# Kernel optimization log

Measured on AMD Instinct MI355X. Metric: run time of the kernel, lower is better.

## Reference

```python
import jax, jax.numpy as jnp
import numpy as np

EPS = 1e-6
ROPE_THETA = 10000.0


def rmsnorm(x, w):
    return x * jax.lax.rsqrt(jnp.mean(x * x, axis=-1, keepdims=True) + EPS) * w


def rope(q, k, seq_len, head_dim):
    # rotate-half RoPE. q,k: [b, h, s, d]
    half = head_dim // 2
    inv_freq = 1.0 / (ROPE_THETA ** (jnp.arange(0, half, dtype=jnp.float32) / half))
    t = jnp.arange(seq_len, dtype=jnp.float32)
    freqs = jnp.outer(t, inv_freq)                      # [s, d/2]
    cos = jnp.concatenate([jnp.cos(freqs)] * 2, axis=-1)  # [s, d]
    sin = jnp.concatenate([jnp.sin(freqs)] * 2, axis=-1)

    def rot(x):
        x1, x2 = x[..., :half], x[..., half:]
        return jnp.concatenate([-x2, x1], axis=-1)

    return q * cos + rot(q) * sin, k * cos + rot(k) * sin


def setup_inputs() -> dict:
    key = jax.random.key(0)
    ks = jax.random.split(key, 8)
    B, S, D, E, F = 4, 2048, 1024, 8, 4096
    sd = 0.02
    return {
        "x": jax.random.normal(ks[0], (B, S, D), dtype=jnp.float32),
        "mapped_tokens": jax.random.randint(ks[1], (B, S), 0, E, dtype=jnp.int32),
        "rms1_w": jnp.ones((D,), dtype=jnp.float32),
        "wqkv": jax.random.normal(ks[2], (D, 3 * D), dtype=jnp.float32) * sd,
        "wo": jax.random.normal(ks[3], (D, D), dtype=jnp.float32) * sd,
        "rms2_w": jnp.ones((D,), dtype=jnp.float32),
        "w1": jax.random.normal(ks[4], (E, D, F), dtype=jnp.float32) * sd,
        "w2": jax.random.normal(ks[5], (E, F, D), dtype=jnp.float32) * sd,
    }


def attention(x, wqkv, wo, num_heads=16):
    B, S, D = x.shape
    hd = D // num_heads
    qkv = x @ wqkv                                       # [b, s, 3D]
    q, k, v = jnp.split(qkv, 3, axis=-1)
    def heads(t):
        return t.reshape(B, S, num_heads, hd).transpose(0, 2, 1, 3)  # [b,h,s,d]
    q, k, v = heads(q), heads(k), heads(v)
    q, k = rope(q, k, S, hd)
    scores = jnp.einsum("bhqd,bhkd->bhqk", q, k) / jnp.sqrt(jnp.float32(hd))
    causal = jnp.tril(jnp.ones((S, S), dtype=bool))
    scores = jnp.where(causal, scores, jnp.finfo(scores.dtype).min)
    attn = jax.nn.softmax(scores, axis=-1)
    out = jnp.einsum("bhqk,bhkd->bhqd", attn, v)
    out = out.transpose(0, 2, 1, 3).reshape(B, S, D)
    return out @ wo


def moe_hash_ffn(x, mapped_tokens, w1, w2):
    # hash-routed MoE: each token goes to exactly one expert given by mapped_tokens
    B, S, D = x.shape
    E = w1.shape[0]
    xf = x.reshape(B * S, D)
    mt = mapped_tokens.reshape(B * S)
    out = jnp.zeros_like(xf)
    for e in range(E):  # small fixed expert count
        y = jax.nn.gelu(xf @ w1[e]) @ w2[e]
        out = out + jnp.where((mt == e)[:, None], y, 0.0)
    return out.reshape(B, S, D)


def reference(x, mapped_tokens, rms1_w, wqkv, wo, rms2_w, w1, w2):
    h = x + attention(rmsnorm(x, rms1_w), wqkv, wo)
    out = h + moe_hash_ffn(rmsnorm(h, rms2_w), mapped_tokens, w1, w2)
    return out
```

## Files before the change

kernel.cpp:

```cpp
#include <hip/hip_runtime.h>
#include <hip/hip_bf16.h>
#include <stdint.h>

typedef __hip_bfloat16 bf16;
typedef __attribute__((ext_vector_type(8))) short bf16x8;
typedef __attribute__((ext_vector_type(4))) float f32x4;
typedef __attribute__((ext_vector_type(16))) float f32x16;
typedef unsigned int u32;

static constexpr int Bsz = 4, S = 2048, D = 1024, E = 8, F = 4096, NH = 16, HD = 64;
static constexpr int TOK = Bsz * S;
static constexpr int SLOTS = TOK + E * 128;

#define DEV __device__ __forceinline__

DEV void async16(const bf16* g, bf16* l) {
  __builtin_amdgcn_global_load_lds((const __attribute__((address_space(1))) u32*)g,
                                   (__attribute__((address_space(3))) u32*)l, 16, 0, 0);
}

DEV u32 lds_off(const bf16* p) {
  return (u32)(uintptr_t)(__attribute__((address_space(3))) bf16*)p;
}

DEV bf16x8 dsr128(u32 addr) {
  bf16x8 d;
  asm volatile("ds_read_b128 %0, %1" : "=v"(d) : "v"(addr));
  return d;
}

DEV float gelu_fast(float x) {
  const float z = 0.7978845608028654f * (x + 0.044715f * x * x * x);
  return x / (1.f + __expf(-2.f * z));
}


__global__ void cvt_transpose(const float* __restrict__ in, bf16* __restrict__ out, int R, int C) {
  __shared__ float t[64][65];
  const size_t zoff = (size_t)blockIdx.z * R * C;
  const int c0 = blockIdx.x * 64, r0 = blockIdx.y * 64;
  const int tid = threadIdx.x;
  const int lrow = tid >> 4, lcol = (tid & 15) * 4;
#pragma unroll
  for (int p = 0; p < 4; ++p) {
    const int r = lrow + p * 16;
    const float4 v = *(const float4*)(in + zoff + (size_t)(r0 + r) * C + c0 + lcol);
    t[r][lcol] = v.x; t[r][lcol + 1] = v.y; t[r][lcol + 2] = v.z; t[r][lcol + 3] = v.w;
  }
  __syncthreads();
  const int ow = tid >> 3, je = (tid & 7) * 8;
#pragma unroll
  for (int p = 0; p < 2; ++p) {
    const int oc = ow + p * 32;
    union { bf16x8 v; bf16 b[8]; } o8;
#pragma unroll
    for (int j = 0; j < 8; ++j) o8.b[j] = __float2bfloat16(t[je + j][oc]);
    *(bf16x8*)(out + zoff + (size_t)(c0 + oc) * R + r0 + je) = o8.v;
  }
}

__global__ void rope_tables(float* __restrict__ cosT, float* __restrict__ sinT) {
  const int s = blockIdx.x * 2 + (threadIdx.x >> 5);
  const int i = threadIdx.x & 31;
  const float inv_freq = powf(10000.f, -(float)i / 32.f);
  const float ang = (float)s * inv_freq;
  cosT[s * 32 + i] = cosf(ang);
  sinT[s * 32 + i] = sinf(ang);
}

__global__ void rmsnorm_k(const float* __restrict__ x, const float* __restrict__ w, bf16* __restrict__ out) {
  const size_t row = blockIdx.x;
  const int tid = threadIdx.x;
  const float4 v = *(const float4*)(x + row * D + tid * 4);
  float ss = v.x * v.x + v.y * v.y + v.z * v.z + v.w * v.w;
#pragma unroll
  for (int off = 1; off < 64; off <<= 1) ss += __shfl_xor(ss, off);
  __shared__ float red[4];
  if ((tid & 63) == 0) red[tid >> 6] = ss;
  __syncthreads();
  const float inv = rsqrtf((red[0] + red[1] + red[2] + red[3]) * (1.f / D) + 1e-6f);
  const float4 wv = *(const float4*)(w + tid * 4);
  union { ushort4 u; bf16 b[4]; } o;
  o.b[0] = __float2bfloat16(v.x * inv * wv.x);
  o.b[1] = __float2bfloat16(v.y * inv * wv.y);
  o.b[2] = __float2bfloat16(v.z * inv * wv.z);
  o.b[3] = __float2bfloat16(v.w * inv * wv.w);
  *(ushort4*)((unsigned short*)out + row * D + tid * 4) = o.u;
}

__global__ void route_init(int* counts, int* cursors, int* perm) {
  const int i = blockIdx.x * 256 + threadIdx.x;
  if (i < E) { counts[i] = 0; cursors[i] = 0; }
  if (i < SLOTS) perm[i] = -1;
}
__global__ void route_count(const int* __restrict__ mt, int* counts) {
  const int i = blockIdx.x * 256 + threadIdx.x;
  if (i < TOK) atomicAdd(&counts[mt[i]], 1);
}
__global__ void route_offsets(const int* __restrict__ counts, int* aoff) {
  if (threadIdx.x == 0) {
    int off = 0; aoff[0] = 0;
    for (int e = 0; e < E; ++e) { off += (counts[e] + 127) & ~127; aoff[e + 1] = off; }
  }
}
__global__ void route_scatter(const int* __restrict__ mt, const int* __restrict__ aoff,
                              int* cursors, int* perm) {
  const int i = blockIdx.x * 256 + threadIdx.x;
  if (i < TOK) { const int e = mt[i]; perm[aoff[e] + atomicAdd(&cursors[e], 1)] = i; }
}

__global__ __launch_bounds__(512) void qkv8p(
    const bf16* __restrict__ A, const bf16* __restrict__ Bt,
    const float* __restrict__ c_t, const float* __restrict__ s_t,
    bf16* __restrict__ o_q, bf16* __restrict__ o_k, bf16* __restrict__ o_v) {
  constexpr int K = 1024, NT = K / 64;
  __shared__ __align__(16) bf16 LA[2][256 * 64];
  __shared__ __align__(16) bf16 LB[2][256 * 64];
  const int tid = threadIdx.x;
  const int lane = tid & 63, wv = tid >> 6;
  const int wm = wv >> 2, wn = wv & 3;
  const int rl = lane & 15, kg = lane >> 4;
  const int gx = gridDim.x;
  const int nwg = gx * gridDim.y;
  int bid = blockIdx.y * gx + blockIdx.x;
  bid = (bid & 7) * (nwg >> 3) + (bid >> 3);
  const int nbase = (bid % gx) * 256, mbase = (bid / gx) * 256;
  f32x4 acc[8][4] = {};
  const int srow = tid >> 3;
  const int sc = (tid & 7) ^ ((srow >> 1) & 7);
  const bf16* Ag = A + (size_t)(mbase + srow) * K + sc * 8;
  const bf16* Bg = Bt + (size_t)(nbase + srow) * K + sc * 8;

  auto stage = [&](int t, int h) {
    const int buf = t & 1;
    const int mat = h >> 1, rh = h & 1;
    const bf16* src = (mat ? Bg : Ag) + (size_t)(rh * 128) * K + t * 64;
    bf16* dst = (mat ? &LB[buf][0] : &LA[buf][0]) + rh * 128 * 64 + tid * 8;
    async16(src, dst);
    async16(src + (size_t)64 * K, dst + 64 * 64);
  };

  bf16x8 bfr[4];
  auto phaseC = [&](int t, int ks, int mih, bool loadB) {
    const int buf = t & 1;
    const u32 ab = lds_off(&LA[buf][0]);
    const u32 bb = lds_off(&LB[buf][0]);
    bf16x8 af[4];
#pragma unroll
    for (int mi = 0; mi < 4; ++mi) {
      const int row = wm * 128 + mih * 64 + mi * 16 + rl;
      const u32 ph = (u32)((ks * 4 + kg) ^ ((row >> 1) & 7));
      af[mi] = dsr128(ab + (u32)row * 128 + ph * 16);
    }
    if (loadB) {
#pragma unroll
      for (int ni = 0; ni < 4; ++ni) {
        const int row = wn * 64 + ni * 16 + rl;
        const u32 ph = (u32)((ks * 4 + kg) ^ ((row >> 1) & 7));
        bfr[ni] = dsr128(bb + (u32)row * 128 + ph * 16);
      }
    }
    asm volatile("s_waitcnt lgkmcnt(0)" ::: "memory");
    __builtin_amdgcn_sched_barrier(0);
    __builtin_amdgcn_s_setprio(1);
#pragma unroll
    for (int mi = 0; mi < 4; ++mi)
#pragma unroll
      for (int ni = 0; ni < 4; ++ni)
        acc[mih * 4 + mi][ni] =
            __builtin_amdgcn_mfma_f32_16x16x32_bf16(af[mi], bfr[ni], acc[mih * 4 + mi][ni], 0, 0, 0);
    __builtin_amdgcn_s_setprio(0);
  };

  stage(0, 0); stage(0, 1); stage(0, 2); stage(0, 3);
  for (int t = 0; t < NT; ++t) {
    const bool more = (t + 1 < NT);
#pragma unroll
    for (int p = 0; p < 4; ++p) {
      if (p == 0) {
        if (more) {
          stage(t + 1, 0);
          asm volatile("s_waitcnt vmcnt(2)" ::: "memory");
        } else {
          asm volatile("s_waitcnt vmcnt(0)" ::: "memory");
        }
        __builtin_amdgcn_s_barrier();
        __builtin_amdgcn_sched_barrier(0);
      } else if (more) {
        stage(t + 1, p);
      }
      phaseC(t, p >> 1, p & 1, (p & 1) == 0);
      __builtin_amdgcn_s_barrier();
      __builtin_amdgcn_sched_barrier(0);
    }
  }

  const int colbase = nbase + wn * 64;
  const int part = colbase >> 10;
  const int head = (colbase & 1023) >> 6;
#pragma unroll
  for (int ai = 0; ai < 8; ++ai) {
    const int rowoff = (ai >> 2) * 64 + (ai & 3) * 16;
#pragma unroll
    for (int r = 0; r < 4; ++r) {
      const int grow = mbase + wm * 128 + rowoff + kg * 4 + r;
      const int bb = grow >> 11, sp = grow & (S - 1);
      if (part == 2) {
#pragma unroll
        for (int ni = 0; ni < 4; ++ni) {
          const int d = ni * 16 + rl;
          o_v[((size_t)(bb * NH + head) * HD + d) * S + sp] = __float2bfloat16(acc[ai][ni][r]);
        }
      } else {
        bf16* dst = (part == 0) ? o_q : o_k;
        const size_t base = ((size_t)(bb * NH + head) * S + sp) * HD;
#pragma unroll
        for (int np = 0; np < 2; ++np) {
          const int i = np * 16 + rl;
          const float c = c_t[sp * 32 + i];
          const float sn = s_t[sp * 32 + i];
          const float lo = acc[ai][np][r];
          const float hi = acc[ai][np + 2][r];
          dst[base + i] = __float2bfloat16(lo * c - hi * sn);
          dst[base + i + 32] = __float2bfloat16(hi * c + lo * sn);
        }
      }
    }
  }
}

template <int EPI, int BM>
__global__ __launch_bounds__(2 * BM) void gemm_bt(
    const bf16* __restrict__ A, const bf16* __restrict__ Bt, int M, int N, int K,
    const int* __restrict__ aoff, long long estride,
    const float* __restrict__ xres, float* __restrict__ o_h,
    bf16* __restrict__ o_act,
    const int* __restrict__ perm, const float* __restrict__ hres, float* __restrict__ o_out) {
  constexpr int WN = BM / 64;
  constexpr int MR = BM / 2;
  constexpr int M_FR = MR / 16;
  __shared__ __align__(16) bf16 As[2][BM * 32];
  __shared__ __align__(16) bf16 Bs[2][BM * 32];
  const int tid = threadIdx.x;
  const int lane = tid & 63, wv = tid >> 6;
  const int wm = wv / WN, wn = wv % WN;
  const int rl = lane & 15, kg = lane >> 4;
  const int gx = gridDim.x;
  const int nwg = gx * gridDim.y;
  int bid = blockIdx.y * gx + blockIdx.x;
  bid = (bid & 7) * (nwg >> 3) + (bid >> 3);
  const int nbase = (bid % gx) * BM, mbase = (bid / gx) * BM;
  const bf16* Btp = Bt;
  if constexpr (EPI >= 2) {
    int e = 0;
#pragma unroll
    for (int t = 0; t < E - 1; ++t) e += (mbase >= aoff[t + 1]) ? 1 : 0;
    Btp = Bt + (size_t)e * estride;
  }
  f32x4 acc[M_FR][4] = {};
  const int srow = tid >> 2;
  const int sc = (tid & 3) ^ ((srow >> 1) & 3);
  const bf16* Agp[2];
#pragma unroll
  for (int c = 0; c < 2; ++c) {
    int rowslot = mbase + c * MR + srow;
    if constexpr (EPI == 2) {
      const int t = perm[rowslot];
      rowslot = (t < 0) ? 0 : t;
    }
    Agp[c] = A + (size_t)rowslot * K + sc * 8;
  }
  const bf16* Bg = Btp + (size_t)(nbase + srow) * K + sc * 8;

  auto stage = [&](int bi, int ko) {
#pragma unroll
    for (int c = 0; c < 2; ++c) {
      async16(Agp[c] + ko, &As[bi][c * MR * 32 + wv * 512]);
      async16(Bg + (size_t)(c * MR) * K + ko, &Bs[bi][c * MR * 32 + wv * 512]);
    }
  };
  auto compute = [&](int bi) {
    bf16x8 af[M_FR], bfr[4];
#pragma unroll
    for (int mi = 0; mi < M_FR; ++mi) {
      const int row = wm * MR + mi * 16 + rl;
      af[mi] = *(const bf16x8*)&As[bi][row * 32 + ((kg ^ ((row >> 1) & 3))) * 8];
    }
#pragma unroll
    for (int ni = 0; ni < 4; ++ni) {
      const int row = wn * 64 + ni * 16 + rl;
      bfr[ni] = *(const bf16x8*)&Bs[bi][row * 32 + ((kg ^ ((row >> 1) & 3))) * 8];
    }
#pragma unroll
    for (int mi = 0; mi < M_FR; ++mi)
#pragma unroll
      for (int ni = 0; ni < 4; ++ni)
        acc[mi][ni] = __builtin_amdgcn_mfma_f32_16x16x32_bf16(af[mi], bfr[ni], acc[mi][ni], 0, 0, 0);
  };

  const int nk = K >> 5;
  stage(0, 0);
  __syncthreads();
  for (int kb = 0; kb < nk; ++kb) {
    if (kb + 1 < nk) stage((kb + 1) & 1, (kb + 1) * 32);
    compute(kb & 1);
    __syncthreads();
  }

#pragma unroll
  for (int mi = 0; mi < M_FR; ++mi) {
#pragma unroll
    for (int ni = 0; ni < 4; ++ni) {
#pragma unroll
      for (int r = 0; r < 4; ++r) {
        const int grow = mbase + wm * MR + mi * 16 + kg * 4 + r;
        const int gcol = nbase + wn * 64 + ni * 16 + rl;
        const float vv = acc[mi][ni][r];
        if constexpr (EPI == 1) {
          const size_t ix = (size_t)grow * 1024 + gcol;
          o_h[ix] = xres[ix] + vv;
        } else if constexpr (EPI == 2) {
          o_act[(size_t)grow * 4096 + gcol] = __float2bfloat16(gelu_fast(vv));
        } else {
          const int t = perm[grow];
          if (t >= 0) {
            const size_t ix = (size_t)t * 1024 + gcol;
            o_out[ix] = hres[ix] + vv;
          }
        }
      }
    }
  }
}

__global__ __launch_bounds__(128, 4) void attn_kernel(const bf16* __restrict__ Qb,
                                                      const bf16* __restrict__ Kb,
                                                      const bf16* __restrict__ Vt,
                                                      bf16* __restrict__ AO) {
  const int bh = blockIdx.x;
  const int w = threadIdx.x >> 6, lane = threadIdx.x & 63;
  const int q = lane & 31, hi = lane >> 5;
  const bf16* Qp = Qb + (size_t)bh * S * HD;
  const bf16* Kp = Kb + (size_t)bh * S * HD;
  const bf16* Vp = Vt + (size_t)bh * S * HD;
  const int b = bh >> 4, h = bh & 15;
  __shared__ __align__(16) bf16 Pl[2][4][32][16];
  const int qt = (S / 32 - 1) - (blockIdx.y * 2 + w);
  const int qrow0 = qt * 32;
  const float SC = 0.125f * 1.4426950408889634f;
  bf16x8 qf[4];
#pragma unroll
  for (int t = 0; t < 4; ++t)
    qf[t] = *(const bf16x8*)(Qp + (size_t)(qrow0 + q) * HD + t * 16 + hi * 8);
  f32x16 oa0 = {}, oa1 = {};
  float m = -INFINITY, l = 0.f;
  const int nt = (qt + 2) >> 1;
  for (int kt = 0; kt < nt; ++kt) {
    const int kvb = kt * 64;
    f32x16 sa0 = {}, sa1 = {};
#pragma unroll
    for (int t = 0; t < 4; ++t) {
      const bf16x8 kf0 = *(const bf16x8*)(Kp + (size_t)(kvb + q) * HD + t * 16 + hi * 8);
      sa0 = __builtin_amdgcn_mfma_f32_32x32x16_bf16(kf0, qf[t], sa0, 0, 0, 0);
    }
#pragma unroll
    for (int t = 0; t < 4; ++t) {
      const bf16x8 kf1 = *(const bf16x8*)(Kp + (size_t)(kvb + 32 + q) * HD + t * 16 + hi * 8);
      sa1 = __builtin_amdgcn_mfma_f32_32x32x16_bf16(kf1, qf[t], sa1, 0, 0, 0);
    }
#pragma unroll
    for (int r = 0; r < 16; ++r) {
      const int kloc = (r & 3) + 8 * (r >> 2) + 4 * hi;
      sa0[r] = (kvb + kloc > qrow0 + q) ? -3.0e38f : sa0[r] * SC;
      sa1[r] = (kvb + 32 + kloc > qrow0 + q) ? -3.0e38f : sa1[r] * SC;
    }
    float vm;
    {
      float a0 = fmaxf(fmaxf(sa0[0], sa0[1]), fmaxf(sa0[2], sa0[3]));
      float a1 = fmaxf(fmaxf(sa0[4], sa0[5]), fmaxf(sa0[6], sa0[7]));
      float a2 = fmaxf(fmaxf(sa0[8], sa0[9]), fmaxf(sa0[10], sa0[11]));
      float a3 = fmaxf(fmaxf(sa0[12], sa0[13]), fmaxf(sa0[14], sa0[15]));
      float b0 = fmaxf(fmaxf(sa1[0], sa1[1]), fmaxf(sa1[2], sa1[3]));
      float b1 = fmaxf(fmaxf(sa1[4], sa1[5]), fmaxf(sa1[6], sa1[7]));
      float b2 = fmaxf(fmaxf(sa1[8], sa1[9]), fmaxf(sa1[10], sa1[11]));
      float b3 = fmaxf(fmaxf(sa1[12], sa1[13]), fmaxf(sa1[14], sa1[15]));
      vm = fmaxf(fmaxf(fmaxf(a0, a1), fmaxf(a2, a3)), fmaxf(fmaxf(b0, b1), fmaxf(b2, b3)));
    }
    vm = fmaxf(vm, __shfl_xor(vm, 32));
    const bool grow = __any(vm > m);
    const float mn = grow ? fmaxf(m, vm) : m;
#pragma unroll
    for (int r = 0; r < 16; ++r) {
      sa0[r] = exp2f(sa0[r] - mn);
      sa1[r] = exp2f(sa1[r] - mn);
    }
    float ps;
    {
      float a0 = (sa0[0] + sa0[1]) + (sa0[2] + sa0[3]);
      float a1 = (sa0[4] + sa0[5]) + (sa0[6] + sa0[7]);
      float a2 = (sa0[8] + sa0[9]) + (sa0[10] + sa0[11]);
      float a3 = (sa0[12] + sa0[13]) + (sa0[14] + sa0[15]);
      float b0 = (sa1[0] + sa1[1]) + (sa1[2] + sa1[3]);
      float b1 = (sa1[4] + sa1[5]) + (sa1[6] + sa1[7]);
      float b2 = (sa1[8] + sa1[9]) + (sa1[10] + sa1[11]);
      float b3 = (sa1[12] + sa1[13]) + (sa1[14] + sa1[15]);
      ps = ((a0 + a1) + (a2 + a3)) + ((b0 + b1) + (b2 + b3));
    }
    ps += __shfl_xor(ps, 32);
    if (grow) {
      const float scs = exp2f(m - mn);
      l = l * scs + ps;
      m = mn;
#pragma unroll
      for (int r = 0; r < 16; ++r) { oa0[r] *= scs; oa1[r] *= scs; }
    } else {
      l += ps;
    }
#pragma unroll
    for (int g = 0; g < 8; ++g) {
      union { ushort4 u4; bf16 bb[4]; } pk;
#pragma unroll
      for (int j = 0; j < 4; ++j) {
        const int r = 4 * (g & 3) + j;
        pk.bb[j] = __float2bfloat16((g < 4) ? sa0[r] : sa1[r]);
      }
      *(ushort4*)&Pl[w][g >> 1][q][8 * (g & 1) + 4 * hi] = pk.u4;
    }
#pragma unroll
    for (int s2i = 0; s2i < 4; ++s2i) {
      const bf16x8 pf = *(const bf16x8*)&Pl[w][s2i][q][8 * hi];
      const bf16x8 vf0 = *(const bf16x8*)(Vp + (size_t)q * S + kvb + 16 * s2i + 8 * hi);
      const bf16x8 vf1 = *(const bf16x8*)(Vp + (size_t)(32 + q) * S + kvb + 16 * s2i + 8 * hi);
      oa0 = __builtin_amdgcn_mfma_f32_32x32x16_bf16(vf0, pf, oa0, 0, 0, 0);
      oa1 = __builtin_amdgcn_mfma_f32_32x32x16_bf16(vf1, pf, oa1, 0, 0, 0);
    }
  }
  const float invl = 1.f / l;
#pragma unroll
  for (int n = 0; n < 2; ++n) {
#pragma unroll
    for (int g = 0; g < 4; ++g) {
      union { ushort4 u4; bf16 bb[4]; } o4;
#pragma unroll
      for (int mi = 0; mi < 4; ++mi) {
        const float val = (n ? oa1[4 * g + mi] : oa0[4 * g + mi]) * invl;
        o4.bb[mi] = __float2bfloat16(val);
      }
      const int d = n * 32 + 8 * g + 4 * hi;
      *(ushort4*)&AO[((size_t)(b * S + qrow0 + q)) * D + h * HD + d] = o4.u4;
    }
  }
}

extern "C" void kernel_launch(void* const* d_in, const int* in_sizes, int n_in,
                              void* d_out, int out_size, void* d_ws, size_t ws_size,
                              hipStream_t stream) {
  const float* x = (const float*)d_in[0];
  const int* mt = (const int*)d_in[1];
  const float* rms1 = (const float*)d_in[2];
  const float* wqkv = (const float*)d_in[3];
  const float* wo = (const float*)d_in[4];
  const float* rms2 = (const float*)d_in[5];
  const float* w1 = (const float*)d_in[6];
  const float* w2 = (const float*)d_in[7];
  float* out = (float*)d_out;
  (void)in_sizes; (void)n_in; (void)out_size; (void)ws_size;

  char* ws = (char*)d_ws;
  size_t off = 0;
  auto alloc = [&](size_t b) { void* p = ws + off; off = (off + b + 255) & ~(size_t)255; return p; };
  bf16* wqkvT = (bf16*)alloc((size_t)3072 * 1024 * 2);
  bf16* woT   = (bf16*)alloc((size_t)1024 * 1024 * 2);
  bf16* w1T   = (bf16*)alloc((size_t)E * F * D * 2);
  bf16* w2T   = (bf16*)alloc((size_t)E * D * F * 2);
  float* cosT = (float*)alloc((size_t)S * 32 * 4);
  float* sinT = (float*)alloc((size_t)S * 32 * 4);
  float* hbuf = (float*)alloc((size_t)TOK * D * 4);
  bf16* xn2   = (bf16*)alloc((size_t)TOK * D * 2);
  int* counts  = (int*)alloc(E * 4);
  int* cursors = (int*)alloc(E * 4);
  int* aoff    = (int*)alloc((E + 1) * 4);
  int* perm    = (int*)alloc(SLOTS * 4);
  char* R = (char*)alloc((size_t)5 * TOK * D * 2);
  bf16* xn = (bf16*)R;
  bf16* qb = (bf16*)(R + (size_t)1 * TOK * D * 2);
  bf16* kb = (bf16*)(R + (size_t)2 * TOK * D * 2);
  bf16* vb = (bf16*)(R + (size_t)3 * TOK * D * 2);
  bf16* ao = (bf16*)(R + (size_t)4 * TOK * D * 2);
  bf16* act = (bf16*)R;

  cvt_transpose<<<dim3(3072 / 64, 1024 / 64, 1), 256, 0, stream>>>(wqkv, wqkvT, 1024, 3072);
  cvt_transpose<<<dim3(1024 / 64, 1024 / 64, 1), 256, 0, stream>>>(wo, woT, 1024, 1024);
  cvt_transpose<<<dim3(4096 / 64, 1024 / 64, E), 256, 0, stream>>>(w1, w1T, 1024, 4096);
  cvt_transpose<<<dim3(1024 / 64, 4096 / 64, E), 256, 0, stream>>>(w2, w2T, 4096, 1024);
  rope_tables<<<dim3(S / 2), 64, 0, stream>>>(cosT, sinT);
  route_init<<<dim3((SLOTS + 255) / 256), 256, 0, stream>>>(counts, cursors, perm);
  route_count<<<dim3(TOK / 256), 256, 0, stream>>>(mt, counts);
  route_offsets<<<dim3(1), 64, 0, stream>>>(counts, aoff);
  route_scatter<<<dim3(TOK / 256), 256, 0, stream>>>(mt, aoff, cursors, perm);
  rmsnorm_k<<<dim3(TOK), 256, 0, stream>>>(x, rms1, xn);
  qkv8p<<<dim3(3072 / 256, TOK / 256), 512, 0, stream>>>(
      xn, wqkvT, cosT, sinT, qb, kb, vb);
  attn_kernel<<<dim3(64, S / 64), 128, 0, stream>>>(qb, kb, vb, ao);
  gemm_bt<1, 128><<<dim3(1024 / 128, TOK / 128), 256, 0, stream>>>(
      ao, woT, TOK, 1024, 1024, nullptr, 0, x, hbuf, nullptr, nullptr, nullptr, nullptr);
  rmsnorm_k<<<dim3(TOK), 256, 0, stream>>>(hbuf, rms2, xn2);
  gemm_bt<2, 128><<<dim3(4096 / 128, SLOTS / 128), 256, 0, stream>>>(
      xn2, w1T, SLOTS, 4096, 1024, aoff, (long long)F * D, nullptr, nullptr, act, perm,
      nullptr, nullptr);
  gemm_bt<3, 128><<<dim3(1024 / 128, SLOTS / 128), 256, 0, stream>>>(
      act, w2T, SLOTS, 1024, 4096, aoff, (long long)D * F, nullptr, nullptr, nullptr, perm,
      hbuf, out);
}
```

Before: 689.3 us.

## Replace MoE FFN GEMMs with 256x256-tile 8-wave pipelined kernel

Adds an ffn4p kernel that computes the expert FFN GEMMs with 256x256 tiles, 512 threads, double-buffered async global-to-LDS loads with swizzled layout, a 4-phase schedule interleaving staging with MFMA, and an XCD-aware block remap. Expert slot padding is raised from 128 to 256 rows to match the larger M tile. The larger tiles aim to improve data reuse and MFMA utilisation. In exchange they add padding waste, use more LDS and registers, and give fewer workgroups.

```diff
diff --git a/kernel.cpp b/kernel.cpp
--- a/kernel.cpp
+++ b/kernel.cpp
@@ -10,7 +10,7 @@
 
 static constexpr int Bsz = 4, S = 2048, D = 1024, E = 8, F = 4096, NH = 16, HD = 64;
 static constexpr int TOK = Bsz * S;
-static constexpr int SLOTS = TOK + E * 128;
+static constexpr int SLOTS = TOK + E * 256;
 
 #define DEV __device__ __forceinline__
 
@@ -100,7 +100,7 @@
 __global__ void route_offsets(const int* __restrict__ counts, int* aoff) {
   if (threadIdx.x == 0) {
     int off = 0; aoff[0] = 0;
-    for (int e = 0; e < E; ++e) { off += (counts[e] + 127) & ~127; aoff[e + 1] = off; }
+    for (int e = 0; e < E; ++e) { off += (counts[e] + 255) & ~255; aoff[e + 1] = off; }
   }
 }
 __global__ void route_scatter(const int* __restrict__ mt, const int* __restrict__ aoff,
@@ -223,6 +223,136 @@
           const float hi = acc[ai][np + 2][r];
           dst[base + i] = __float2bfloat16(lo * c - hi * sn);
           dst[base + i + 32] = __float2bfloat16(hi * c + lo * sn);
+        }
+      }
+    }
+  }
+}
+
+template <int EPI, int K>
+__global__ __launch_bounds__(512) void ffn4p(
+    const bf16* __restrict__ A, const bf16* __restrict__ Bt,
+    const int* __restrict__ aoff, long long estride,
+    bf16* __restrict__ o_act,
+    const int* __restrict__ perm, const float* __restrict__ hres,
+    float* __restrict__ o_out) {
+  constexpr int NT = K / 64;
+  __shared__ __align__(16) bf16 LA[2][256 * 64];
+  __shared__ __align__(16) bf16 LB[2][256 * 64];
+  const int tid = threadIdx.x;
+  const int lane = tid & 63, wv = tid >> 6;
+  const int wm = wv >> 2, wn = wv & 3;
+  const int rl = lane & 15, kg = lane >> 4;
+  const int gx = gridDim.x;
+  const int nwg = gx * gridDim.y;
+  int bid = blockIdx.y * gx + blockIdx.x;
+  bid = (bid & 7) * (nwg >> 3) + (bid >> 3);
+  const int nbase = (bid % gx) * 256, mbase = (bid / gx) * 256;
+  if (mbase >= aoff[E]) return;
+  int e = 0;
+#pragma unroll
+  for (int t = 0; t < E - 1; ++t) e += (mbase >= aoff[t + 1]) ? 1 : 0;
+  const bf16* Btp = Bt + (size_t)e * estride;
+
+  f32x4 acc[8][4] = {};
+  const int srow = tid >> 3;
+  const int sc = (tid & 7) ^ ((srow >> 1) & 7);
+  const bf16* Agr[4];
+#pragma unroll
+  for (int c = 0; c < 4; ++c) {
+    int slot = mbase + c * 64 + srow;
+    if constexpr (EPI == 2) { const int pt = perm[slot]; slot = (pt < 0) ? 0 : pt; }
+    Agr[c] = A + (size_t)slot * K + sc * 8;
+  }
+  const bf16* Bg = Btp + (size_t)(nbase + srow) * K + sc * 8;
+
+  auto stage = [&](int t, int h) {
+    const int buf = t & 1;
+    const int mat = h >> 1, rh = h & 1;
+    bf16* dst = (mat ? &LB[buf][0] : &LA[buf][0]) + rh * 128 * 64 + tid * 8;
+    if (mat == 0) {
+      async16(Agr[rh * 2] + t * 64, dst);
+      async16(Agr[rh * 2 + 1] + t * 64, dst + 64 * 64);
+    } else {
+      const bf16* src = Bg + (size_t)(rh * 128) * K + t * 64;
+      async16(src, dst);
+      async16(src + (size_t)64 * K, dst + 64 * 64);
+    }
+  };
+
+  bf16x8 bfr[4];
+  auto phaseC = [&](int t, int ks, int mih, bool loadB) {
+    const int buf = t & 1;
+    const u32 ab = lds_off(&LA[buf][0]);
+    const u32 bb = lds_off(&LB[buf][0]);
+    bf16x8 af[4];
+#pragma unroll
+    for (int mi = 0; mi < 4; ++mi) {
+      const int row = wm * 128 + mih * 64 + mi * 16 + rl;
+      const u32 ph = (u32)((ks * 4 + kg) ^ ((row >> 1) & 7));
+      af[mi] = dsr128(ab + (u32)row * 128 + ph * 16);
+    }
+    if (loadB) {
+#pragma unroll
+      for (int ni = 0; ni < 4; ++ni) {
+        const int row = wn * 64 + ni * 16 + rl;
+        const u32 ph = (u32)((ks * 4 + kg) ^ ((row >> 1) & 7));
+        bfr[ni] = dsr128(bb + (u32)row * 128 + ph * 16);
+      }
+    }
+    asm volatile("s_waitcnt lgkmcnt(0)" ::: "memory");
+    __builtin_amdgcn_sched_barrier(0);
+    __builtin_amdgcn_s_setprio(1);
+#pragma unroll
+    for (int mi = 0; mi < 4; ++mi)
+#pragma unroll
+      for (int ni = 0; ni < 4; ++ni)
+        acc[mih * 4 + mi][ni] =
+            __builtin_amdgcn_mfma_f32_16x16x32_bf16(af[mi], bfr[ni], acc[mih * 4 + mi][ni], 0, 0, 0);
+    __builtin_amdgcn_s_setprio(0);
+  };
+
+  stage(0, 0); stage(0, 1); stage(0, 2); stage(0, 3);
+  for (int t = 0; t < NT; ++t) {
+    const bool more = (t + 1 < NT);
+#pragma unroll
+    for (int p = 0; p < 4; ++p) {
+      if (p == 0) {
+        if (more) {
+          stage(t + 1, 0);
+          asm volatile("s_waitcnt vmcnt(2)" ::: "memory");
+        } else {
+          asm volatile("s_waitcnt vmcnt(0)" ::: "memory");
+        }
+        __builtin_amdgcn_s_barrier();
+        __builtin_amdgcn_sched_barrier(0);
+      } else if (more) {
+        stage(t + 1, p);
+      }
+      phaseC(t, p >> 1, p & 1, (p & 1) == 0);
+      __builtin_amdgcn_s_barrier();
+      __builtin_amdgcn_sched_barrier(0);
+    }
+  }
+
+#pragma unroll
+  for (int ai = 0; ai < 8; ++ai) {
+    const int rowoff = (ai >> 2) * 64 + (ai & 3) * 16;
+#pragma unroll
+    for (int r = 0; r < 4; ++r) {
+      const int grow = mbase + wm * 128 + rowoff + kg * 4 + r;
+#pragma unroll
+      for (int ni = 0; ni < 4; ++ni) {
+        const int gcol = nbase + wn * 64 + ni * 16 + rl;
+        const float vv = acc[ai][ni][r];
+        if constexpr (EPI == 2) {
+          o_act[(size_t)grow * 4096 + gcol] = __float2bfloat16(gelu_fast(vv));
+        } else {
+          const int tk = perm[grow];
+          if (tk >= 0) {
+            const size_t ix = (size_t)tk * 1024 + gcol;
+            o_out[ix] = hres[ix] + vv;
+          }
         }
       }
     }
@@ -505,10 +635,8 @@
   gemm_bt<1, 128><<<dim3(1024 / 128, TOK / 128), 256, 0, stream>>>(
       ao, woT, TOK, 1024, 1024, nullptr, 0, x, hbuf, nullptr, nullptr, nullptr, nullptr);
   rmsnorm_k<<<dim3(TOK), 256, 0, stream>>>(hbuf, rms2, xn2);
-  gemm_bt<2, 128><<<dim3(4096 / 128, SLOTS / 128), 256, 0, stream>>>(
-      xn2, w1T, SLOTS, 4096, 1024, aoff, (long long)F * D, nullptr, nullptr, act, perm,
-      nullptr, nullptr);
-  gemm_bt<3, 128><<<dim3(1024 / 128, SLOTS / 128), 256, 0, stream>>>(
-      act, w2T, SLOTS, 1024, 4096, aoff, (long long)D * F, nullptr, nullptr, nullptr, perm,
-      hbuf, out);
-}
+  ffn4p<2, 1024><<<dim3(4096 / 256, SLOTS / 256), 512, 0, stream>>>(
+      xn2, w1T, aoff, (long long)F * D, act, perm, nullptr, nullptr);
+  ffn4p<3, 4096><<<dim3(1024 / 256, SLOTS / 256), 512, 0, stream>>>(
+      act, w2T, aoff, (long long)D * F, nullptr, perm, hbuf, out);
+}
```

After: 708.4 us. 2.8% more time.

## Register-level P transpose, K prefetch, and folded softmax scale in attention

Applied to the files above, without the earlier changes.

Folds the 1/sqrt(d)*log2e softmax scale into Q at the QKV GEMM epilogue, so the attention loop no longer multiplies every score. The causal mask is now applied only on diagonal tiles. K for the next tile is prefetched into registers and V loads are issued early. The P matrix is repacked to bf16 with v_cvt_pk and v_permlane32_swap instead of a round trip through LDS. These changes raise register pressure, which the launch bound lowers from 4 to 3 waves, and they add rounding from scaling Q before the bf16 conversion.

```diff
diff --git a/kernel.cpp b/kernel.cpp
--- a/kernel.cpp
+++ b/kernel.cpp
@@ -32,6 +32,12 @@
 DEV float gelu_fast(float x) {
   const float z = 0.7978845608028654f * (x + 0.044715f * x * x * x);
   return x / (1.f + __expf(-2.f * z));
+}
+
+DEV u32 cvtpk(float lo, float hi) {
+  u32 r;
+  asm("v_cvt_pk_bf16_f32 %0, %1, %2" : "=v"(r) : "v"(lo), "v"(hi));
+  return r;
 }
 
 
@@ -198,6 +204,7 @@
   const int colbase = nbase + wn * 64;
   const int part = colbase >> 10;
   const int head = (colbase & 1023) >> 6;
+  const float qs = (part == 0) ? 0.18033688011112042f : 1.f;
 #pragma unroll
   for (int ai = 0; ai < 8; ++ai) {
     const int rowoff = (ai >> 2) * 64 + (ai & 3) * 16;
@@ -221,8 +228,8 @@
           const float sn = s_t[sp * 32 + i];
           const float lo = acc[ai][np][r];
           const float hi = acc[ai][np + 2][r];
-          dst[base + i] = __float2bfloat16(lo * c - hi * sn);
-          dst[base + i + 32] = __float2bfloat16(hi * c + lo * sn);
+          dst[base + i] = __float2bfloat16((lo * c - hi * sn) * qs);
+          dst[base + i + 32] = __float2bfloat16((hi * c + lo * sn) * qs);
         }
       }
     }
@@ -333,7 +340,7 @@
   }
 }
 
-__global__ __launch_bounds__(128, 4) void attn_kernel(const bf16* __restrict__ Qb,
+__global__ __launch_bounds__(128, 3) void attn_kernel(const bf16* __restrict__ Qb,
                                                       const bf16* __restrict__ Kb,
                                                       const bf16* __restrict__ Vt,
                                                       bf16* __restrict__ AO) {
@@ -344,10 +351,8 @@
   const bf16* Kp = Kb + (size_t)bh * S * HD;
   const bf16* Vp = Vt + (size_t)bh * S * HD;
   const int b = bh >> 4, h = bh & 15;
-  __shared__ __align__(16) bf16 Pl[2][4][32][16];
   const int qt = (S / 32 - 1) - (blockIdx.y * 2 + w);
   const int qrow0 = qt * 32;
-  const float SC = 0.125f * 1.4426950408889634f;
   bf16x8 qf[4];
 #pragma unroll
   for (int t = 0; t < 4; ++t)
@@ -355,24 +360,48 @@
   f32x16 oa0 = {}, oa1 = {};
   float m = -INFINITY, l = 0.f;
   const int nt = (qt + 2) >> 1;
+
+  bf16x8 kf[8];
+  auto loadK = [&](int kvb) {
+#pragma unroll
+    for (int t = 0; t < 4; ++t) {
+      kf[t]     = *(const bf16x8*)(Kp + (size_t)(kvb + q) * HD + t * 16 + hi * 8);
+      kf[4 + t] = *(const bf16x8*)(Kp + (size_t)(kvb + 32 + q) * HD + t * 16 + hi * 8);
+    }
+  };
+  auto packP = [&](float s0, float s1, float s2, float s3,
+                   float s4, float s5, float s6, float s7) -> bf16x8 {
+    u32 x0 = cvtpk(s0, s1), x1 = cvtpk(s2, s3);
+    u32 y0 = cvtpk(s4, s5), y1 = cvtpk(s6, s7);
+    asm volatile("v_permlane32_swap_b32 %0, %1" : "+v"(x0), "+v"(y0));
+    asm volatile("v_permlane32_swap_b32 %0, %1" : "+v"(x1), "+v"(y1));
+    union { u32 w[4]; bf16x8 v; } u;
+    u.w[0] = x0; u.w[1] = x1; u.w[2] = y0; u.w[3] = y1;
+    return u.v;
+  };
+
+  loadK(0);
   for (int kt = 0; kt < nt; ++kt) {
     const int kvb = kt * 64;
     f32x16 sa0 = {}, sa1 = {};
 #pragma unroll
-    for (int t = 0; t < 4; ++t) {
-      const bf16x8 kf0 = *(const bf16x8*)(Kp + (size_t)(kvb + q) * HD + t * 16 + hi * 8);
-      sa0 = __builtin_amdgcn_mfma_f32_32x32x16_bf16(kf0, qf[t], sa0, 0, 0, 0);
-    }
-#pragma unroll
-    for (int t = 0; t < 4; ++t) {
-      const bf16x8 kf1 = *(const bf16x8*)(Kp + (size_t)(kvb + 32 + q) * HD + t * 16 + hi * 8);
-      sa1 = __builtin_amdgcn_mfma_f32_32x32x16_bf16(kf1, qf[t], sa1, 0, 0, 0);
-    }
-#pragma unroll
-    for (int r = 0; r < 16; ++r) {
-      const int kloc = (r & 3) + 8 * (r >> 2) + 4 * hi;
-      sa0[r] = (kvb + kloc > qrow0 + q) ? -3.0e38f : sa0[r] * SC;
-      sa1[r] = (kvb + 32 + kloc > qrow0 + q) ? -3.0e38f : sa1[r] * SC;
+    for (int t = 0; t < 4; ++t) sa0 = __builtin_amdgcn_mfma_f32_32x32x16_bf16(kf[t], qf[t], sa0, 0, 0, 0);
+#pragma unroll
+    for (int t = 0; t < 4; ++t) sa1 = __builtin_amdgcn_mfma_f32_32x32x16_bf16(kf[4 + t], qf[t], sa1, 0, 0, 0);
+    bf16x8 vf0[4], vf1[4];
+#pragma unroll
+    for (int s2i = 0; s2i < 4; ++s2i) {
+      vf0[s2i] = *(const bf16x8*)(Vp + (size_t)q * S + kvb + 16 * s2i + 8 * hi);
+      vf1[s2i] = *(const bf16x8*)(Vp + (size_t)(32 + q) * S + kvb + 16 * s2i + 8 * hi);
+    }
+    if (kt + 1 < nt) loadK(kvb + 64);
+    if (kvb + 63 > qrow0) {
+#pragma unroll
+      for (int r = 0; r < 16; ++r) {
+        const int kloc = (r & 3) + 8 * (r >> 2) + 4 * hi;
+        sa0[r] = (kvb + kloc > qrow0 + q) ? -3.0e38f : sa0[r];
+        sa1[r] = (kvb + 32 + kloc > qrow0 + q) ? -3.0e38f : sa1[r];
+      }
     }
     float vm;
     {
@@ -416,23 +445,19 @@
     } else {
       l += ps;
     }
-#pragma unroll
-    for (int g = 0; g < 8; ++g) {
-      union { ushort4 u4; bf16 bb[4]; } pk;
-#pragma unroll
-      for (int j = 0; j < 4; ++j) {
-        const int r = 4 * (g & 3) + j;
-        pk.bb[j] = __float2bfloat16((g < 4) ? sa0[r] : sa1[r]);
-      }
-      *(ushort4*)&Pl[w][g >> 1][q][8 * (g & 1) + 4 * hi] = pk.u4;
-    }
-#pragma unroll
-    for (int s2i = 0; s2i < 4; ++s2i) {
-      const bf16x8 pf = *(const bf16x8*)&Pl[w][s2i][q][8 * hi];
-      const bf16x8 vf0 = *(const bf16x8*)(Vp + (size_t)q * S + kvb + 16 * s2i + 8 * hi);
-      const bf16x8 vf1 = *(const bf16x8*)(Vp + (size_t)(32 + q) * S + kvb + 16 * s2i + 8 * hi);
-      oa0 = __builtin_amdgcn_mfma_f32_32x32x16_bf16(vf0, pf, oa0, 0, 0, 0);
-      oa1 = __builtin_amdgcn_mfma_f32_32x32x16_bf16(vf1, pf, oa1, 0, 0, 0);
+    {
+      const bf16x8 pf0 = packP(sa0[0], sa0[1], sa0[2], sa0[3], sa0[4], sa0[5], sa0[6], sa0[7]);
+      oa0 = __builtin_amdgcn_mfma_f32_32x32x16_bf16(vf0[0], pf0, oa0, 0, 0, 0);
+      oa1 = __builtin_amdgcn_mfma_f32_32x32x16_bf16(vf1[0], pf0, oa1, 0, 0, 0);
+      const bf16x8 pf1 = packP(sa0[8], sa0[9], sa0[10], sa0[11], sa0[12], sa0[13], sa0[14], sa0[15]);
+      oa0 = __builtin_amdgcn_mfma_f32_32x32x16_bf16(vf0[1], pf1, oa0, 0, 0, 0);
+      oa1 = __builtin_amdgcn_mfma_f32_32x32x16_bf16(vf1[1], pf1, oa1, 0, 0, 0);
+      const bf16x8 pf2 = packP(sa1[0], sa1[1], sa1[2], sa1[3], sa1[4], sa1[5], sa1[6], sa1[7]);
+      oa0 = __builtin_amdgcn_mfma_f32_32x32x16_bf16(vf0[2], pf2, oa0, 0, 0, 0);
+      oa1 = __builtin_amdgcn_mfma_f32_32x32x16_bf16(vf1[2], pf2, oa1, 0, 0, 0);
+      const bf16x8 pf3 = packP(sa1[8], sa1[9], sa1[10], sa1[11], sa1[12], sa1[13], sa1[14], sa1[15]);
+      oa0 = __builtin_amdgcn_mfma_f32_32x32x16_bf16(vf0[3], pf3, oa0, 0, 0, 0);
+      oa1 = __builtin_amdgcn_mfma_f32_32x32x16_bf16(vf1[3], pf3, oa1, 0, 0, 0);
     }
   }
   const float invl = 1.f / l;
```

After: 698.6 us. About the same (+1.4%).
